# Kernel optimization log

Measured on AMD Instinct MI355X. Metric: run time of the kernel, lower is better.

The kernel has to match this reference:

```python
import jax, jax.numpy as jnp
import numpy as np

B, N, E, F, H, K, C, G = 64, 2048, 16384, 32, 64, 8, 16, 64


def setup_inputs() -> dict:
    key = jax.random.key(0)
    ks = jax.random.split(key, 10)
    s = lambda fan: 1.0 / np.sqrt(fan)
    return {
        "x": jax.random.normal(ks[0], (B, N, C), jnp.float32),
        "linc": (jax.random.uniform(ks[1], (N, E)) < (8.0 / N)).astype(jnp.float32),
        "rinc": (jax.random.uniform(ks[2], (E, N)) < (8.0 / N)).astype(jnp.float32),
        "ef": jax.random.normal(ks[3], (E, F), jnp.float32),
        "w1": jax.random.uniform(ks[4], (H, F), jnp.float32, -s(F), s(F)),
        "b1": jax.random.uniform(ks[5], (H,), jnp.float32, -s(F), s(F)),
        "w2": jax.random.uniform(ks[6], (K, H), jnp.float32, -s(H), s(H)),
        "b2": jax.random.uniform(ks[7], (K,), jnp.float32, -s(H), s(H)),
        "gcw": jax.random.uniform(ks[8], (G, C * K), jnp.float32, -s(C * K), s(C * K)),
        "gcb": jax.random.uniform(ks[9], (G,), jnp.float32, -s(C * K), s(C * K)),
    }


def reference(x, linc, rinc, ef, w1, b1, w2, b2, gcw, gcb):
    # edge MLP -> per-edge kernel weights [E, K]
    h = jax.nn.relu(ef @ w1.T + b1)
    w = h @ w2.T + b2
    # structurally: y_k = linc @ diag(w[:,k]) @ rinc @ x, without building [K,N,N]
    z = jnp.einsum('en,bnc->bec', rinc, x)                  # gather: node -> edge
    y = jnp.einsum('ne,ek,bec->bnck', linc, w, z)           # scale + scatter: edge -> node
    b = x.shape[0]
    y = y.reshape(b, N, C * K)                              # matches permute(0,2,-1,1).reshape
    out = jax.nn.relu(y @ gcw.T + gcb)                      # [B, N, G]
    return out.reshape(b, -1)
```

## Files before the change

kernel.cpp:

```cpp
#include <hip/hip_runtime.h>
#include <hip/hip_bf16.h>

#define B_ 64
#define N_ 2048
#define E_ 16384
#define F_ 32
#define H_ 64
#define K_ 8
#define C_ 16
#define G_ 64
#define CK 128
#define CAP 128
#define YLD 136
#define BC 1024

typedef __attribute__((ext_vector_type(8))) short bf16x8;
typedef __attribute__((ext_vector_type(4))) float f32x4;

__device__ inline float bf2f(unsigned short u) {
  union { unsigned int i; float f; } v; v.i = ((unsigned int)u) << 16; return v.f;
}
__device__ inline unsigned short f2bf(float f) {
  union { float f; unsigned int i; } v; v.f = f;
  unsigned int x = v.i;
  return (unsigned short)((x + 0x7fffu + ((x >> 16) & 1u)) >> 16);
}

__global__ __launch_bounds__(256) void xpose_k(
    const float* __restrict__ x, unsigned short* __restrict__ x_t) {
  int t = threadIdx.x;
  int n = blockIdx.x;
  int b = t >> 2, c0 = (t & 3) * 4;
  float4 xv = *(const float4*)(x + (size_t)b*(N_*C_) + (size_t)n*C_ + c0);
  ushort4 o;
  o.x = f2bf(xv.x); o.y = f2bf(xv.y); o.z = f2bf(xv.z); o.w = f2bf(xv.w);
  *(ushort4*)&x_t[(size_t)n*BC + 4*t] = o;
}

__global__ __launch_bounds__(256) void edge_mlp_k(
    const float* __restrict__ ef, const float* __restrict__ w1,
    const float* __restrict__ b1, const float* __restrict__ w2,
    const float* __restrict__ b2, float* __restrict__ w_out) {
  __shared__ float s_w1[H_*F_];
  __shared__ float s_w2[K_*H_];
  __shared__ float s_b1[H_];
  __shared__ float s_b2[K_];
  int t = threadIdx.x;
  for (int i = t; i < H_*F_; i += 256) s_w1[i] = w1[i];
  for (int i = t; i < K_*H_; i += 256) s_w2[i] = w2[i];
  if (t < H_) s_b1[t] = b1[t];
  if (t < K_) s_b2[t] = b2[t];
  __syncthreads();
  int e = blockIdx.x*256 + t;
  float efr[F_];
  const float4* efp = (const float4*)(ef + (size_t)e*F_);
  #pragma unroll
  for (int f4 = 0; f4 < F_/4; f4++) {
    float4 v = efp[f4];
    efr[f4*4+0]=v.x; efr[f4*4+1]=v.y; efr[f4*4+2]=v.z; efr[f4*4+3]=v.w;
  }
  float acc[K_];
  #pragma unroll
  for (int k = 0; k < K_; k++) acc[k] = s_b2[k];
  #pragma unroll 4
  for (int h = 0; h < H_; h++) {
    float hv = s_b1[h];
    #pragma unroll
    for (int f = 0; f < F_; f++) hv = fmaf(efr[f], s_w1[h*F_+f], hv);
    hv = fmaxf(hv, 0.f);
    #pragma unroll
    for (int k = 0; k < K_; k++) acc[k] = fmaf(hv, s_w2[k*H_+h], acc[k]);
  }
  #pragma unroll
  for (int k = 0; k < K_; k++) w_out[(size_t)e*K_ + k] = acc[k];
}

__global__ __launch_bounds__(256) void gather_z_k(
    const float* __restrict__ rinc, const unsigned short* __restrict__ x_t,
    unsigned short* __restrict__ z) {
  __shared__ int s_idx[64];
  __shared__ int s_cnt;
  int t = threadIdx.x;
  int e = blockIdx.x;
  if (t == 0) s_cnt = 0;
  __syncthreads();
  const float4* row = (const float4*)(rinc + (size_t)e*N_);
  #pragma unroll
  for (int j = 0; j < N_/4/256; j++) {
    int i = t + 256*j;
    float4 v = row[i];
    if (v.x != 0.f) { int p = atomicAdd(&s_cnt,1); if (p<64) s_idx[p]=i*4+0; }
    if (v.y != 0.f) { int p = atomicAdd(&s_cnt,1); if (p<64) s_idx[p]=i*4+1; }
    if (v.z != 0.f) { int p = atomicAdd(&s_cnt,1); if (p<64) s_idx[p]=i*4+2; }
    if (v.w != 0.f) { int p = atomicAdd(&s_cnt,1); if (p<64) s_idx[p]=i*4+3; }
  }
  __syncthreads();
  int cnt = min(s_cnt, 64);
  const unsigned short* xt = x_t + 4*t;
  float4 acc = make_float4(0.f, 0.f, 0.f, 0.f);
  for (int i = 0; i < cnt; i++) {
    int n = s_idx[i];
    ushort4 xv = *(const ushort4*)(xt + (size_t)n*BC);
    acc.x += bf2f(xv.x); acc.y += bf2f(xv.y); acc.z += bf2f(xv.z); acc.w += bf2f(xv.w);
  }
  ushort4 zu;
  zu.x = f2bf(acc.x); zu.y = f2bf(acc.y); zu.z = f2bf(acc.z); zu.w = f2bf(acc.w);
  *(ushort4*)&z[(size_t)e*BC + 4*t] = zu;
}

__global__ __launch_bounds__(256, 4) void node_out_k(
    const float* __restrict__ linc, const unsigned short* __restrict__ z,
    const float* __restrict__ w, const float* __restrict__ gcw,
    const float* __restrict__ gcb, float* __restrict__ out) {
  __shared__ unsigned short s_y[B_*YLD];
  __shared__ unsigned short s_gcwB[G_*YLD];
  __shared__ float s_gcb[G_];
  __shared__ int   s_idx[CAP];
  __shared__ float s_w[CAP*K_];
  __shared__ int   s_cnt;
  int t = threadIdx.x;
  int n = blockIdx.x;
  if (t == 0) s_cnt = 0;
  __syncthreads();

  for (int i = t; i < G_*CK; i += 256) {
    int g = i >> 7, ck = i & (CK-1);
    s_gcwB[g*YLD + ck] = f2bf(gcw[i]);
  }
  if (t < G_) s_gcb[t] = gcb[t];

  const float4* row = (const float4*)(linc + (size_t)n*E_);
  #pragma unroll
  for (int j = 0; j < E_/4/256; j++) {
    int i = t + 256*j;
    float4 v = row[i];
    if (v.x != 0.f) { int p = atomicAdd(&s_cnt,1); if (p<CAP) s_idx[p]=i*4+0; }
    if (v.y != 0.f) { int p = atomicAdd(&s_cnt,1); if (p<CAP) s_idx[p]=i*4+1; }
    if (v.z != 0.f) { int p = atomicAdd(&s_cnt,1); if (p<CAP) s_idx[p]=i*4+2; }
    if (v.w != 0.f) { int p = atomicAdd(&s_cnt,1); if (p<CAP) s_idx[p]=i*4+3; }
  }
  __syncthreads();
  int cnt = min(s_cnt, CAP);
  for (int i = t; i < cnt*K_; i += 256) {
    int ii = i >> 3, k = i & 7;
    s_w[i] = w[(size_t)s_idx[ii]*K_ + k];
  }
  __syncthreads();

  float acc[4][K_];
  #pragma unroll
  for (int j = 0; j < 4; j++)
    #pragma unroll
    for (int k = 0; k < K_; k++) acc[j][k] = 0.f;
  const unsigned short* zt = z + 4*t;
  for (int i = 0; i < cnt; i++) {
    int e = s_idx[i];
    const float4* wp = (const float4*)&s_w[i*K_];
    float4 w0 = wp[0], w1v = wp[1];
    float we[K_] = {w0.x, w0.y, w0.z, w0.w, w1v.x, w1v.y, w1v.z, w1v.w};
    ushort4 zu = *(const ushort4*)(zt + (size_t)e*BC);
    float zv[4] = {bf2f(zu.x), bf2f(zu.y), bf2f(zu.z), bf2f(zu.w)};
    #pragma unroll
    for (int j = 0; j < 4; j++)
      #pragma unroll
      for (int k = 0; k < K_; k++) acc[j][k] = fmaf(zv[j], we[k], acc[j][k]);
  }
  {
    int b = t >> 2, ckb = (t & 3) * 32;
    #pragma unroll
    for (int j = 0; j < 4; j++) {
      ushort4 lo, hi;
      lo.x = f2bf(acc[j][0]); lo.y = f2bf(acc[j][1]); lo.z = f2bf(acc[j][2]); lo.w = f2bf(acc[j][3]);
      hi.x = f2bf(acc[j][4]); hi.y = f2bf(acc[j][5]); hi.z = f2bf(acc[j][6]); hi.w = f2bf(acc[j][7]);
      *(ushort4*)&s_y[b*YLD + ckb + 8*j]     = lo;
      *(ushort4*)&s_y[b*YLD + ckb + 8*j + 4] = hi;
    }
  }
  __syncthreads();

  {
    int wv = t >> 6, lane = t & 63;
    int m = lane & 15, q = lane >> 4;
    f32x4 cf0 = {0.f,0.f,0.f,0.f}, cf1 = cf0, cf2 = cf0, cf3 = cf0;
    #pragma unroll
    for (int ks = 0; ks < 4; ks++) {
      bf16x8 a = *(const bf16x8*)&s_y[(16*wv + m)*YLD + 32*ks + 8*q];
      bf16x8 b0 = *(const bf16x8*)&s_gcwB[(m     )*YLD + 32*ks + 8*q];
      bf16x8 b1 = *(const bf16x8*)&s_gcwB[(16 + m)*YLD + 32*ks + 8*q];
      bf16x8 b2 = *(const bf16x8*)&s_gcwB[(32 + m)*YLD + 32*ks + 8*q];
      bf16x8 b3 = *(const bf16x8*)&s_gcwB[(48 + m)*YLD + 32*ks + 8*q];
      cf0 = __builtin_amdgcn_mfma_f32_16x16x32_bf16(a, b0, cf0, 0, 0, 0);
      cf1 = __builtin_amdgcn_mfma_f32_16x16x32_bf16(a, b1, cf1, 0, 0, 0);
      cf2 = __builtin_amdgcn_mfma_f32_16x16x32_bf16(a, b2, cf2, 0, 0, 0);
      cf3 = __builtin_amdgcn_mfma_f32_16x16x32_bf16(a, b3, cf3, 0, 0, 0);
    }
    float* ob = out + (size_t)n*G_;
    #pragma unroll
    for (int r = 0; r < 4; r++) {
      int b = 16*wv + 4*q + r;
      float* op = ob + (size_t)b*(N_*G_);
      float v0 = fmaxf(cf0[r] + s_gcb[m],      0.f);
      float v1 = fmaxf(cf1[r] + s_gcb[16 + m], 0.f);
      float v2 = fmaxf(cf2[r] + s_gcb[32 + m], 0.f);
      float v3 = fmaxf(cf3[r] + s_gcb[48 + m], 0.f);
      op[m]      = v0;
      op[16 + m] = v1;
      op[32 + m] = v2;
      op[48 + m] = v3;
    }
  }
}

extern "C" void kernel_launch(void* const* d_in, const int* in_sizes, int n_in,
                              void* d_out, int out_size, void* d_ws, size_t ws_size,
                              hipStream_t stream) {
  const float* x    = (const float*)d_in[0];
  const float* linc = (const float*)d_in[1];
  const float* rinc = (const float*)d_in[2];
  const float* ef   = (const float*)d_in[3];
  const float* w1   = (const float*)d_in[4];
  const float* b1   = (const float*)d_in[5];
  const float* w2   = (const float*)d_in[6];
  const float* b2   = (const float*)d_in[7];
  const float* gcw  = (const float*)d_in[8];
  const float* gcb  = (const float*)d_in[9];
  float* out = (float*)d_out;

  char* ws = (char*)d_ws;
  float* w_e          = (float*)ws;                 ws += (size_t)E_*K_*sizeof(float);
  unsigned short* z   = (unsigned short*)ws;        ws += (size_t)E_*BC*sizeof(short);
  unsigned short* x_t = (unsigned short*)ws;        ws += (size_t)N_*BC*sizeof(short);

  xpose_k<<<N_, 256, 0, stream>>>(x, x_t);
  edge_mlp_k<<<E_/256, 256, 0, stream>>>(ef, w1, b1, w2, b2, w_e);
  gather_z_k<<<E_, 256, 0, stream>>>(rinc, x_t, z);
  node_out_k<<<N_, 256, 0, stream>>>(linc, z, w_e, gcw, gcb, out);
}
```

Baseline: 373.0 us.

## Use one wave per edge in gather, shrink node kernel LDS for occupancy

The gather kernel now processes four edges per block, one per wavefront, so it needs no block-wide barriers, and each lane handles 16 contiguous bf16 values with wider loads. The node-output kernel drops its LDS copy of gcw and reads gcw from global memory straight into MFMA operands. It also stores edge weights as bf16 and lowers CAP, cutting LDS use so occupancy can rise to 8 blocks per CU. The trade-offs are extra precision loss in the edge weights, repeated global reads of gcw per wave, and lower caps on neighbor counts. The gather kernel reads s_cnt after the atomics without a barrier, relying on the wave executing in lockstep.

```diff
diff --git a/kernel.cpp b/kernel.cpp
--- a/kernel.cpp
+++ b/kernel.cpp
@@ -10,11 +10,13 @@
 #define C_ 16
 #define G_ 64
 #define CK 128
-#define CAP 128
+#define CAP 120
+#define RCAP 72
 #define YLD 136
 #define BC 1024
 
 typedef __attribute__((ext_vector_type(8))) short bf16x8;
+typedef __attribute__((ext_vector_type(8))) unsigned short u16x8;
 typedef __attribute__((ext_vector_type(4))) float f32x4;
 
 __device__ inline float bf2f(unsigned short u) {
@@ -78,56 +80,55 @@
 __global__ __launch_bounds__(256) void gather_z_k(
     const float* __restrict__ rinc, const unsigned short* __restrict__ x_t,
     unsigned short* __restrict__ z) {
-  __shared__ int s_idx[64];
-  __shared__ int s_cnt;
-  int t = threadIdx.x;
-  int e = blockIdx.x;
-  if (t == 0) s_cnt = 0;
-  __syncthreads();
+  __shared__ int s_idx[4][RCAP];
+  __shared__ int s_cnt[4];
+  int t = threadIdx.x, wv = t >> 6, lane = t & 63;
+  int e = blockIdx.x * 4 + wv;
+  if (lane == 0) s_cnt[wv] = 0;
   const float4* row = (const float4*)(rinc + (size_t)e*N_);
   #pragma unroll
-  for (int j = 0; j < N_/4/256; j++) {
-    int i = t + 256*j;
+  for (int j = 0; j < N_/4/64; j++) {
+    int i = lane + 64*j;
     float4 v = row[i];
-    if (v.x != 0.f) { int p = atomicAdd(&s_cnt,1); if (p<64) s_idx[p]=i*4+0; }
-    if (v.y != 0.f) { int p = atomicAdd(&s_cnt,1); if (p<64) s_idx[p]=i*4+1; }
-    if (v.z != 0.f) { int p = atomicAdd(&s_cnt,1); if (p<64) s_idx[p]=i*4+2; }
-    if (v.w != 0.f) { int p = atomicAdd(&s_cnt,1); if (p<64) s_idx[p]=i*4+3; }
-  }
-  __syncthreads();
-  int cnt = min(s_cnt, 64);
-  const unsigned short* xt = x_t + 4*t;
-  float4 acc = make_float4(0.f, 0.f, 0.f, 0.f);
+    if (v.x != 0.f) { int p = atomicAdd(&s_cnt[wv],1); if (p<RCAP) s_idx[wv][p]=i*4+0; }
+    if (v.y != 0.f) { int p = atomicAdd(&s_cnt[wv],1); if (p<RCAP) s_idx[wv][p]=i*4+1; }
+    if (v.z != 0.f) { int p = atomicAdd(&s_cnt[wv],1); if (p<RCAP) s_idx[wv][p]=i*4+2; }
+    if (v.w != 0.f) { int p = atomicAdd(&s_cnt[wv],1); if (p<RCAP) s_idx[wv][p]=i*4+3; }
+  }
+  int cnt = min(s_cnt[wv], RCAP);
+  const unsigned short* xb = x_t + 16*lane;
+  float acc[16];
+  #pragma unroll
+  for (int k = 0; k < 16; k++) acc[k] = 0.f;
   for (int i = 0; i < cnt; i++) {
-    int n = s_idx[i];
-    ushort4 xv = *(const ushort4*)(xt + (size_t)n*BC);
-    acc.x += bf2f(xv.x); acc.y += bf2f(xv.y); acc.z += bf2f(xv.z); acc.w += bf2f(xv.w);
-  }
-  ushort4 zu;
-  zu.x = f2bf(acc.x); zu.y = f2bf(acc.y); zu.z = f2bf(acc.z); zu.w = f2bf(acc.w);
-  *(ushort4*)&z[(size_t)e*BC + 4*t] = zu;
-}
-
-__global__ __launch_bounds__(256, 4) void node_out_k(
+    int n = s_idx[wv][i];
+    u16x8 a0 = *(const u16x8*)(xb + (size_t)n*BC);
+    u16x8 a1 = *(const u16x8*)(xb + (size_t)n*BC + 8);
+    #pragma unroll
+    for (int k = 0; k < 8; k++) { acc[k] += bf2f(a0[k]); acc[8+k] += bf2f(a1[k]); }
+  }
+  u16x8 o0, o1;
+  #pragma unroll
+  for (int k = 0; k < 8; k++) { o0[k] = f2bf(acc[k]); o1[k] = f2bf(acc[8+k]); }
+  unsigned short* zp = z + (size_t)e*BC + 16*lane;
+  *(u16x8*)zp = o0;
+  *(u16x8*)(zp + 8) = o1;
+}
+
+__global__ __launch_bounds__(256, 8) void node_out_k(
     const float* __restrict__ linc, const unsigned short* __restrict__ z,
     const float* __restrict__ w, const float* __restrict__ gcw,
     const float* __restrict__ gcb, float* __restrict__ out) {
   __shared__ unsigned short s_y[B_*YLD];
-  __shared__ unsigned short s_gcwB[G_*YLD];
+  __shared__ unsigned short s_wb[CAP*K_];
   __shared__ float s_gcb[G_];
   __shared__ int   s_idx[CAP];
-  __shared__ float s_w[CAP*K_];
   __shared__ int   s_cnt;
   int t = threadIdx.x;
   int n = blockIdx.x;
   if (t == 0) s_cnt = 0;
-  __syncthreads();
-
-  for (int i = t; i < G_*CK; i += 256) {
-    int g = i >> 7, ck = i & (CK-1);
-    s_gcwB[g*YLD + ck] = f2bf(gcw[i]);
-  }
   if (t < G_) s_gcb[t] = gcb[t];
+  __syncthreads();
 
   const float4* row = (const float4*)(linc + (size_t)n*E_);
   #pragma unroll
@@ -143,7 +144,7 @@
   int cnt = min(s_cnt, CAP);
   for (int i = t; i < cnt*K_; i += 256) {
     int ii = i >> 3, k = i & 7;
-    s_w[i] = w[(size_t)s_idx[ii]*K_ + k];
+    s_wb[i] = f2bf(w[(size_t)s_idx[ii]*K_ + k]);
   }
   __syncthreads();
 
@@ -155,9 +156,10 @@
   const unsigned short* zt = z + 4*t;
   for (int i = 0; i < cnt; i++) {
     int e = s_idx[i];
-    const float4* wp = (const float4*)&s_w[i*K_];
-    float4 w0 = wp[0], w1v = wp[1];
-    float we[K_] = {w0.x, w0.y, w0.z, w0.w, w1v.x, w1v.y, w1v.z, w1v.w};
+    u16x8 wv8 = *(const u16x8*)&s_wb[i*K_];
+    float we[K_];
+    #pragma unroll
+    for (int k = 0; k < K_; k++) we[k] = bf2f(wv8[k]);
     ushort4 zu = *(const ushort4*)(zt + (size_t)e*BC);
     float zv[4] = {bf2f(zu.x), bf2f(zu.y), bf2f(zu.z), bf2f(zu.w)};
     #pragma unroll
@@ -185,14 +187,21 @@
     #pragma unroll
     for (int ks = 0; ks < 4; ks++) {
       bf16x8 a = *(const bf16x8*)&s_y[(16*wv + m)*YLD + 32*ks + 8*q];
-      bf16x8 b0 = *(const bf16x8*)&s_gcwB[(m     )*YLD + 32*ks + 8*q];
-      bf16x8 b1 = *(const bf16x8*)&s_gcwB[(16 + m)*YLD + 32*ks + 8*q];
-      bf16x8 b2 = *(const bf16x8*)&s_gcwB[(32 + m)*YLD + 32*ks + 8*q];
-      bf16x8 b3 = *(const bf16x8*)&s_gcwB[(48 + m)*YLD + 32*ks + 8*q];
-      cf0 = __builtin_amdgcn_mfma_f32_16x16x32_bf16(a, b0, cf0, 0, 0, 0);
-      cf1 = __builtin_amdgcn_mfma_f32_16x16x32_bf16(a, b1, cf1, 0, 0, 0);
-      cf2 = __builtin_amdgcn_mfma_f32_16x16x32_bf16(a, b2, cf2, 0, 0, 0);
-      cf3 = __builtin_amdgcn_mfma_f32_16x16x32_bf16(a, b3, cf3, 0, 0, 0);
+      bf16x8 bf[4];
+      #pragma unroll
+      for (int gf = 0; gf < 4; gf++) {
+        const float* gp = gcw + (size_t)(16*gf + m)*CK + 32*ks + 8*q;
+        float4 g0 = *(const float4*)gp;
+        float4 g1 = *(const float4*)(gp + 4);
+        bf[gf][0]=(short)f2bf(g0.x); bf[gf][1]=(short)f2bf(g0.y);
+        bf[gf][2]=(short)f2bf(g0.z); bf[gf][3]=(short)f2bf(g0.w);
+        bf[gf][4]=(short)f2bf(g1.x); bf[gf][5]=(short)f2bf(g1.y);
+        bf[gf][6]=(short)f2bf(g1.z); bf[gf][7]=(short)f2bf(g1.w);
+      }
+      cf0 = __builtin_amdgcn_mfma_f32_16x16x32_bf16(a, bf[0], cf0, 0, 0, 0);
+      cf1 = __builtin_amdgcn_mfma_f32_16x16x32_bf16(a, bf[1], cf1, 0, 0, 0);
+      cf2 = __builtin_amdgcn_mfma_f32_16x16x32_bf16(a, bf[2], cf2, 0, 0, 0);
+      cf3 = __builtin_amdgcn_mfma_f32_16x16x32_bf16(a, bf[3], cf3, 0, 0, 0);
     }
     float* ob = out + (size_t)n*G_;
     #pragma unroll
@@ -233,6 +242,6 @@
 
   xpose_k<<<N_, 256, 0, stream>>>(x, x_t);
   edge_mlp_k<<<E_/256, 256, 0, stream>>>(ef, w1, b1, w2, b2, w_e);
-  gather_z_k<<<E_, 256, 0, stream>>>(rinc, x_t, z);
+  gather_z_k<<<E_/4, 256, 0, stream>>>(rinc, x_t, z);
   node_out_k<<<N_, 256, 0, stream>>>(linc, z, w_e, gcw, gcb, out);
 }
```

Result: slower. 398.5 us (+6.8%).
